# Performance work log

Measured on AMD Instinct MI355X. Metric: run time of the kernel, lower is better.

## Reference

```python
import jax, jax.numpy as jnp
import numpy as np

N_NODES = 16000
N_EDGES = 256000
DIM = 256
HEADS = 8
DH = DIM // HEADS
BLOCKS = 3
EPS = 1e-5


def _ln_graph(x, g, b):
    # PyG LayerNorm, mode='graph', batch=None: scalar mean/std over ALL elements,
    # then per-channel affine.
    x = x - x.mean()
    x = x / (x.std() + EPS)
    return x * g + b


def _block(x, src, dst, x_edge, inv_dist, p):
    (Wq, bq, Wk, bk, Wv, bv, We, Ws, bs, g1, b1, W1, c1, W2, c2, g2, b2) = p
    # per-edge gather + projections  [E, H, DH]
    q = (x[dst] @ Wq + bq).reshape(N_EDGES, HEADS, DH)
    e = (x_edge @ We).reshape(N_EDGES, HEADS, DH)          # lin_edge (no bias)
    k = (x[src] @ Wk + bk).reshape(N_EDGES, HEADS, DH) + e
    # distance-scaled attention logits [E, H]
    alpha = (q * k).sum(-1) * (inv_dist[:, None] / np.sqrt(DH))
    # segment softmax over destination nodes (PyG softmax, +1e-16 in denom)
    amax = jax.ops.segment_max(alpha, dst, num_segments=N_NODES)
    ex = jnp.exp(alpha - amax[dst])
    denom = jax.ops.segment_sum(ex, dst, num_segments=N_NODES)
    attn = ex / (denom[dst] + 1e-16)
    v = (x[src] @ Wv + bv).reshape(N_EDGES, HEADS, DH) + e
    msg = (v * attn[:, :, None]).reshape(N_EDGES, DIM)      # concat heads
    out = jax.ops.segment_sum(msg, dst, num_segments=N_NODES)
    out = out + x @ Ws + bs                                 # root / skip weight
    x = _ln_graph(x + out, g1, b1)                          # mha residual + norm
    ffn = jnp.maximum(x @ W1 + c1, 0.0) @ W2 + c2           # 2-layer ReLU MLP
    return _ln_graph(x + ffn, g2, b2)


def setup_inputs() -> dict:
    key = jax.random.key(0)
    ks = jax.random.split(key, 16)
    s = 0.05
    B = BLOCKS

    def w(k, shape):
        return jax.random.normal(k, shape, jnp.float32) * s

    return {
        'x': jax.random.normal(ks[0], (N_NODES, DIM), jnp.float32),
        'edge_index': jax.random.randint(ks[1], (2, N_EDGES), 0, N_NODES),
        'x_edge': jax.random.normal(ks[2], (N_EDGES, DIM), jnp.float32),
        'x_dist': jax.random.uniform(ks[3], (N_EDGES,), jnp.float32, 1.0, 5.0),
        'Wq': w(ks[4], (B, DIM, DIM)), 'bq': jnp.zeros((B, DIM), jnp.float32),
        'Wk': w(ks[5], (B, DIM, DIM)), 'bk': jnp.zeros((B, DIM), jnp.float32),
        'Wv': w(ks[6], (B, DIM, DIM)), 'bv': jnp.zeros((B, DIM), jnp.float32),
        'We': w(ks[7], (B, DIM, DIM)),
        'Wskip': w(ks[8], (B, DIM, DIM)), 'bskip': jnp.zeros((B, DIM), jnp.float32),
        'ln1_g': jnp.ones((B, DIM), jnp.float32), 'ln1_b': jnp.zeros((B, DIM), jnp.float32),
        'W1': w(ks[9], (B, DIM, 4 * DIM)), 'bf1': jnp.zeros((B, 4 * DIM), jnp.float32),
        'W2': w(ks[10], (B, 4 * DIM, DIM)), 'bf2': jnp.zeros((B, DIM), jnp.float32),
        'ln2_g': jnp.ones((B, DIM), jnp.float32), 'ln2_b': jnp.zeros((B, DIM), jnp.float32),
    }


def reference(x, edge_index, x_edge, x_dist, Wq, bq, Wk, bk, Wv, bv, We,
              Wskip, bskip, ln1_g, ln1_b, W1, bf1, W2, bf2, ln2_g, ln2_b):
    src, dst = edge_index[0], edge_index[1]  # PyG: x_j = x[src], x_i = x[dst]
    inv_dist = 1.0 / x_dist
    for i in range(BLOCKS):
        p = (Wq[i], bq[i], Wk[i], bk[i], Wv[i], bv[i], We[i], Wskip[i], bskip[i],
             ln1_g[i], ln1_b[i], W1[i], bf1[i], W2[i], bf2[i], ln2_g[i], ln2_b[i])
        x = _block(x, src, dst, x_edge, inv_dist, p)
    return x
```

## Files before the change

kernel.cpp:

```cpp
#include <hip/hip_runtime.h>
#include <hip/hip_bf16.h>
#include <cstddef>

#define N_NODES 16000
#define N_EDGES 256000
#define DIM 256
#define HEADS 8
#define DFF 1024
#define LN_EPS 1e-5f
#define CNT ((float)((size_t)N_NODES * DIM))
#define RSDH 0.17677669529663687f

typedef __attribute__((ext_vector_type(8))) short short8;
typedef __attribute__((ext_vector_type(4))) float floatx4;

__device__ __forceinline__ float bf2f(unsigned int s) {
    return __uint_as_float(s << 16);
}

__device__ __forceinline__ float2 ln_ms(const float* __restrict__ s) {
    float mu = s[0] * (1.0f / CNT);
    float var = s[1] * (1.0f / CNT) - mu * mu;
    float2 r; r.x = mu; r.y = 1.0f / (sqrtf(fmaxf(var, 0.0f)) + LN_EPS);
    return r;
}

__device__ __forceinline__ void async16(const __hip_bfloat16* g, __hip_bfloat16* l) {
    __builtin_amdgcn_global_load_lds(
        (const __attribute__((address_space(1))) void*)g,
        (__attribute__((address_space(3))) void*)l, 16, 0, 0);
}

__device__ __forceinline__ void pack8(__hip_bfloat16* d, float4 a, float4 b) {
    union { short8 f; __hip_bfloat16 h[8]; } u;
    u.h[0] = __float2bfloat16(a.x); u.h[1] = __float2bfloat16(a.y);
    u.h[2] = __float2bfloat16(a.z); u.h[3] = __float2bfloat16(a.w);
    u.h[4] = __float2bfloat16(b.x); u.h[5] = __float2bfloat16(b.y);
    u.h[6] = __float2bfloat16(b.z); u.h[7] = __float2bfloat16(b.w);
    *(short8*)d = u.f;
}

__device__ __forceinline__ float4 lnaff(float4 v, float4 g, float4 b, float mu, float sc) {
    v.x = (v.x - mu) * sc * g.x + b.x;
    v.y = (v.y - mu) * sc * g.y + b.y;
    v.z = (v.z - mu) * sc * g.z + b.z;
    v.w = (v.w - mu) * sc * g.w + b.w;
    return v;
}

template<int BIAS, int RELU, int RES, int OBF16, int ACVT, int TM>
__global__ __launch_bounds__(256) void mgemm_k(
    const void* __restrict__ Ap, const __hip_bfloat16* __restrict__ Bt,
    const float* __restrict__ bias, const float* __restrict__ res,
    void* __restrict__ C, int M, int K, int N,
    const float* __restrict__ lnA_s, const float* __restrict__ lnA_g,
    const float* __restrict__ lnA_b,
    const float* __restrict__ lnR_s, const float* __restrict__ lnR_g,
    const float* __restrict__ lnR_b,
    float* __restrict__ ostats)
{
    __shared__ __hip_bfloat16 As[TM * 32];
    __shared__ __hip_bfloat16 Bs[128 * 32];
    __shared__ float rs[8];
    const int tid = threadIdx.x;
    const int lane = tid & 63, wv = tid >> 6;
    const int wm = (TM == 128) ? (wv & 1) * 64 : 0;
    const int wn = (TM == 128) ? (wv >> 1) * 64 : wv * 32;
    const int NJ = (TM == 128) ? 4 : 2;
    const int row0 = blockIdx.y * TM, col0 = blockIdx.x * 128;
    const int lr = tid >> 2;
    const int lk = (tid & 3) * 8;

    float muA = 0.0f, scA = 1.0f;
    if (ACVT && lnA_s) { float2 t = ln_ms(lnA_s); muA = t.x; scA = t.y; }

    floatx4 acc[4][4];
    const floatx4 zf = {0.f, 0.f, 0.f, 0.f};
    #pragma unroll
    for (int i = 0; i < 4; i++)
        #pragma unroll
        for (int j = 0; j < 4; j++) acc[i][j] = zf;

    const int a_fo = (wm + (lane & 15)) * 32 + (lane >> 4) * 8;
    const int b_fo = (wn + (lane & 15)) * 32 + (lane >> 4) * 8;

    for (int k0 = 0; k0 < K; k0 += 32) {
        if (ACVT) {
            const float* A = (const float*)Ap;
            const float* p0 = A + (size_t)(row0 + lr) * K + k0 + lk;
            float4 v0 = *(const float4*)(p0);
            float4 v1 = *(const float4*)(p0 + 4);
            if (lnA_s) {
                float4 ga = *(const float4*)(lnA_g + k0 + lk);
                float4 gb = *(const float4*)(lnA_g + k0 + lk + 4);
                float4 ba = *(const float4*)(lnA_b + k0 + lk);
                float4 bb = *(const float4*)(lnA_b + k0 + lk + 4);
                v0 = lnaff(v0, ga, ba, muA, scA);
                v1 = lnaff(v1, gb, bb, muA, scA);
                if (TM == 128) {
                    const float* p1 = A + (size_t)(row0 + lr + 64) * K + k0 + lk;
                    float4 w0 = lnaff(*(const float4*)(p1), ga, ba, muA, scA);
                    float4 w1 = lnaff(*(const float4*)(p1 + 4), gb, bb, muA, scA);
                    pack8(As + 2048 + tid * 8, w0, w1);
                }
            } else if (TM == 128) {
                const float* p1 = A + (size_t)(row0 + lr + 64) * K + k0 + lk;
                pack8(As + 2048 + tid * 8, *(const float4*)(p1), *(const float4*)(p1 + 4));
            }
            pack8(As + tid * 8, v0, v1);
        } else {
            const __hip_bfloat16* A = (const __hip_bfloat16*)Ap;
            async16(A + (size_t)(row0 + lr) * K + k0 + lk, As + tid * 8);
            if (TM == 128)
                async16(A + (size_t)(row0 + lr + 64) * K + k0 + lk, As + 2048 + tid * 8);
        }
        async16(Bt + (size_t)(col0 + lr) * K + k0 + lk, Bs + tid * 8);
        async16(Bt + (size_t)(col0 + lr + 64) * K + k0 + lk, Bs + 2048 + tid * 8);
        __syncthreads();
        short8 a[4], b[4];
        #pragma unroll
        for (int i = 0; i < 4; i++)
            a[i] = *(const short8*)(As + a_fo + i * 16 * 32);
        #pragma unroll
        for (int j = 0; j < NJ; j++)
            b[j] = *(const short8*)(Bs + b_fo + j * 16 * 32);
        #pragma unroll
        for (int i = 0; i < 4; i++)
            #pragma unroll
            for (int j = 0; j < NJ; j++)
                acc[i][j] = __builtin_amdgcn_mfma_f32_16x16x32_bf16(a[i], b[j], acc[i][j], 0, 0, 0);
        __syncthreads();
    }
    float muR = 0.0f, scR = 1.0f;
    if (RES && lnR_s) { float2 t = ln_ms(lnR_s); muR = t.x; scR = t.y; }
    const int rbase = row0 + wm + (lane >> 4) * 4;
    const int cbase = col0 + wn + (lane & 15);
    float s1 = 0.0f, s2 = 0.0f;
    #pragma unroll
    for (int j = 0; j < NJ; j++) {
        const int c = cbase + j * 16;
        float bb = BIAS ? bias[c] : 0.0f;
        float gr = (RES && lnR_s) ? lnR_g[c] : 1.0f;
        float br = (RES && lnR_s) ? lnR_b[c] : 0.0f;
        #pragma unroll
        for (int i = 0; i < 4; i++) {
            #pragma unroll
            for (int r = 0; r < 4; r++) {
                const int rr = rbase + i * 16 + r;
                float v = acc[i][j][r] + bb;
                if (RELU) v = fmaxf(v, 0.0f);
                if (RES) {
                    float rv = res[(size_t)rr * N + c];
                    if (lnR_s) rv = (rv - muR) * scR * gr + br;
                    v += rv;
                }
                if (ostats) { s1 += v; s2 += v * v; }
                if (OBF16 == 2) {
                    const int cc = c & 255;
                    const int idx = ((cc >> 2) << 3) + (cc & 3) + ((c >> 8) << 2);
                    ((__hip_bfloat16*)C)[(size_t)rr * N + idx] = __float2bfloat16(v);
                } else if (OBF16) {
                    ((__hip_bfloat16*)C)[(size_t)rr * N + c] = __float2bfloat16(v);
                } else {
                    ((float*)C)[(size_t)rr * N + c] = v;
                }
            }
        }
    }
    if (ostats) {
        #pragma unroll
        for (int o = 32; o > 0; o >>= 1) {
            s1 += __shfl_down(s1, o);
            s2 += __shfl_down(s2, o);
        }
        if (lane == 0) { rs[wv] = s1; rs[4 + wv] = s2; }
        __syncthreads();
        if (tid == 0) {
            atomicAdd(&ostats[0], rs[0] + rs[1] + rs[2] + rs[3]);
            atomicAdd(&ostats[1], rs[4] + rs[5] + rs[6] + rs[7]);
        }
    }
}

__global__ __launch_bounds__(256) void tcvt_k(const float* __restrict__ src,
                                              __hip_bfloat16* __restrict__ dst,
                                              int R, int C, int sStride, int dStride)
{
    src += (size_t)blockIdx.z * sStride;
    dst += (size_t)blockIdx.z * dStride;
    __shared__ float t[32][33];
    const int c0 = blockIdx.x * 32, r0 = blockIdx.y * 32;
    const int tx = threadIdx.x & 31, ty = threadIdx.x >> 5;
    #pragma unroll
    for (int j = 0; j < 32; j += 8)
        t[ty + j][tx] = src[(size_t)(r0 + ty + j) * C + c0 + tx];
    __syncthreads();
    #pragma unroll
    for (int j = 0; j < 32; j += 8)
        dst[(size_t)(c0 + ty + j) * R + r0 + tx] = __float2bfloat16(t[tx][ty + j]);
}

__global__ __launch_bounds__(256) void bcat_k(const float* __restrict__ ba,
                                              const float* __restrict__ bb,
                                              const float* __restrict__ bc,
                                              const float* __restrict__ bd,
                                              float* __restrict__ o)
{
    const int z = blockIdx.y;
    int t = blockIdx.x * 256 + threadIdx.x;
    float v = (t < 256) ? ba[z * 256 + t] : (t < 512) ? bb[z * 256 + t - 256]
            : (t < 768) ? bc[z * 256 + t - 512] : bd[z * 256 + t - 768];
    o[(size_t)z * 1024 + t] = v;
}

__global__ __launch_bounds__(256) void hist_k(const int* __restrict__ dst, int* __restrict__ deg)
{
    int e = blockIdx.x * blockDim.x + threadIdx.x;
    if (e < N_EDGES) atomicAdd(&deg[dst[e]], 1);
}

__global__ __launch_bounds__(1024) void scan_k(const int* __restrict__ deg,
                                               int* __restrict__ rowptr,
                                               int* __restrict__ cursor)
{
    __shared__ int wsum[16];
    const int t = threadIdx.x;
    const int base = t * 16;
    int local[16];
    int s = 0;
    if (t < 1000) {
        #pragma unroll
        for (int j = 0; j < 16; j++) { local[j] = s; s += deg[base + j]; }
    }
    const int lane = t & 63, w = t >> 6;
    int v = s;
    #pragma unroll
    for (int off = 1; off < 64; off <<= 1) {
        int u = __shfl_up(v, off);
        if (lane >= off) v += u;
    }
    if (lane == 63) wsum[w] = v;
    __syncthreads();
    if (t == 0) {
        int r = 0;
        #pragma unroll
        for (int i = 0; i < 16; i++) { int u = wsum[i]; wsum[i] = r; r += u; }
    }
    __syncthreads();
    const int excl = v - s + wsum[w];
    if (t < 1000) {
        #pragma unroll
        for (int j = 0; j < 16; j++) {
            rowptr[base + j] = excl + local[j];
            cursor[base + j] = excl + local[j];
        }
        if (t == 999) rowptr[16000] = excl + s;
    }
}

__global__ __launch_bounds__(256) void scatter_k(const int* __restrict__ dst,
                                                 const int* __restrict__ src,
                                                 const float* __restrict__ xd,
                                                 int* __restrict__ cursor,
                                                 int* __restrict__ eperm,
                                                 int* __restrict__ srcp,
                                                 float* __restrict__ scale)
{
    int e = blockIdx.x * blockDim.x + threadIdx.x;
    if (e < N_EDGES) {
        int pos = atomicAdd(&cursor[dst[e]], 1);
        eperm[pos] = e;
        srcp[pos] = src[e];
        scale[pos] = RSDH / xd[e];
    }
}

__global__ __launch_bounds__(256) void eprep_k(const float* __restrict__ xe,
                                               const int* __restrict__ eperm,
                                               __hip_bfloat16* __restrict__ xeb)
{
    const int r = blockIdx.x * 4 + (threadIdx.x >> 6);
    const int lane = threadIdx.x & 63;
    const int e = eperm[r];
    float4 v = *(const float4*)(xe + (size_t)e * DIM + lane * 4);
    union { short4 s; __hip_bfloat16 h[4]; } u;
    u.h[0] = __float2bfloat16(v.x); u.h[1] = __float2bfloat16(v.y);
    u.h[2] = __float2bfloat16(v.z); u.h[3] = __float2bfloat16(v.w);
    *(short4*)(xeb + (size_t)r * DIM + lane * 4) = u.s;
}

__global__ __launch_bounds__(256) void node_agg_k(
    const float* __restrict__ qs, const __hip_bfloat16* __restrict__ kvb,
    const __hip_bfloat16* __restrict__ Ep,
    const int* __restrict__ srcp, const float* __restrict__ scale,
    const int* __restrict__ rowptr,
    const float* __restrict__ xsrc, const float* __restrict__ lnx_s,
    const float* __restrict__ lnx_g, const float* __restrict__ lnx_b,
    float* __restrict__ y, float* __restrict__ ostats)
{
    __shared__ float rs[8];
    const int lane = threadIdx.x & 63;
    const int wv = threadIdx.x >> 6;
    const int n = blockIdx.x * 4 + wv;
    const float4 q = *(const float4*)(qs + (size_t)n * 512 + lane * 4);
    float aA0 = 0, aA1 = 0, aA2 = 0, aA3 = 0, denA = 0;
    float aB0 = 0, aB1 = 0, aB2 = 0, aB3 = 0, denB = 0;
    const int beg = rowptr[n], end = rowptr[n + 1];
    int i = beg;
    int sC = (i + 2 < end) ? srcp[i + 2] : 0;
    int sD = (i + 3 < end) ? srcp[i + 3] : 0;
    uint4 kvA = {0, 0, 0, 0}, kvB = {0, 0, 0, 0};
    uint2 ebA = {0, 0}, ebB = {0, 0};
    float scA = 0.f, scB = 0.f;
    if (i < end) {
        const int sA = srcp[i];
        kvA = *(const uint4*)(kvb + (size_t)sA * 512 + lane * 8);
        ebA = *(const uint2*)(Ep + (size_t)i * DIM + lane * 4);
        scA = scale[i];
    }
    if (i + 1 < end) {
        const int sB = srcp[i + 1];
        kvB = *(const uint4*)(kvb + (size_t)sB * 512 + lane * 8);
        ebB = *(const uint2*)(Ep + (size_t)(i + 1) * DIM + lane * 4);
        scB = scale[i + 1];
    }
    while (i + 1 < end) {
        const uint4 kA = kvA, kB = kvB;
        const uint2 eA = ebA, eB = ebB;
        const float cA = scA, cB = scB;
        if (i + 2 < end) {
            kvA = *(const uint4*)(kvb + (size_t)sC * 512 + lane * 8);
            ebA = *(const uint2*)(Ep + (size_t)(i + 2) * DIM + lane * 4);
            scA = scale[i + 2];
            sC = (i + 4 < end) ? srcp[i + 4] : 0;
        }
        if (i + 3 < end) {
            kvB = *(const uint4*)(kvb + (size_t)sD * 512 + lane * 8);
            ebB = *(const uint2*)(Ep + (size_t)(i + 3) * DIM + lane * 4);
            scB = scale[i + 3];
            sD = (i + 5 < end) ? srcp[i + 5] : 0;
        }
        const float eA0 = bf2f(eA.x & 0xffffu), eA1 = bf2f(eA.x >> 16);
        const float eA2 = bf2f(eA.y & 0xffffu), eA3 = bf2f(eA.y >> 16);
        const float eB0 = bf2f(eB.x & 0xffffu), eB1 = bf2f(eB.x >> 16);
        const float eB2 = bf2f(eB.y & 0xffffu), eB3 = bf2f(eB.y >> 16);
        float pA = q.x * (bf2f(kA.x & 0xffffu) + eA0)
                 + q.y * (bf2f(kA.x >> 16) + eA1)
                 + q.z * (bf2f(kA.y & 0xffffu) + eA2)
                 + q.w * (bf2f(kA.y >> 16) + eA3);
        float pB = q.x * (bf2f(kB.x & 0xffffu) + eB0)
                 + q.y * (bf2f(kB.x >> 16) + eB1)
                 + q.z * (bf2f(kB.y & 0xffffu) + eB2)
                 + q.w * (bf2f(kB.y >> 16) + eB3);
        pA += __shfl_xor(pA, 1); pB += __shfl_xor(pB, 1);
        pA += __shfl_xor(pA, 2); pB += __shfl_xor(pB, 2);
        pA += __shfl_xor(pA, 4); pB += __shfl_xor(pB, 4);
        const float exA = __expf(pA * cA);
        const float exB = __expf(pB * cB);
        denA += exA; denB += exB;
        aA0 = fmaf(bf2f(kA.z & 0xffffu) + eA0, exA, aA0);
        aA1 = fmaf(bf2f(kA.z >> 16) + eA1, exA, aA1);
        aA2 = fmaf(bf2f(kA.w & 0xffffu) + eA2, exA, aA2);
        aA3 = fmaf(bf2f(kA.w >> 16) + eA3, exA, aA3);
        aB0 = fmaf(bf2f(kB.z & 0xffffu) + eB0, exB, aB0);
        aB1 = fmaf(bf2f(kB.z >> 16) + eB1, exB, aB1);
        aB2 = fmaf(bf2f(kB.w & 0xffffu) + eB2, exB, aB2);
        aB3 = fmaf(bf2f(kB.w >> 16) + eB3, exB, aB3);
        i += 2;
    }
    if (i < end) {
        const float e0 = bf2f(ebA.x & 0xffffu), e1 = bf2f(ebA.x >> 16);
        const float e2 = bf2f(ebA.y & 0xffffu), e3 = bf2f(ebA.y >> 16);
        float pA = q.x * (bf2f(kvA.x & 0xffffu) + e0)
                 + q.y * (bf2f(kvA.x >> 16) + e1)
                 + q.z * (bf2f(kvA.y & 0xffffu) + e2)
                 + q.w * (bf2f(kvA.y >> 16) + e3);
        pA += __shfl_xor(pA, 1);
        pA += __shfl_xor(pA, 2);
        pA += __shfl_xor(pA, 4);
        const float ex = __expf(pA * scA);
        denA += ex;
        aA0 = fmaf(bf2f(kvA.z & 0xffffu) + e0, ex, aA0);
        aA1 = fmaf(bf2f(kvA.z >> 16) + e1, ex, aA1);
        aA2 = fmaf(bf2f(kvA.w & 0xffffu) + e2, ex, aA2);
        aA3 = fmaf(bf2f(kvA.w >> 16) + e3, ex, aA3);
    }
    const float dn = 1.0f / (denA + denB + 1e-16f);
    const float a0 = aA0 + aB0, a1 = aA1 + aB1, a2 = aA2 + aB2, a3 = aA3 + aB3;
    const size_t o = (size_t)n * DIM + lane * 4;
    float4 xr = *(const float4*)(xsrc + o);
    if (lnx_s) {
        float2 t = ln_ms(lnx_s);
        const float4 g4 = *(const float4*)(lnx_g + lane * 4);
        const float4 b4 = *(const float4*)(lnx_b + lane * 4);
        xr = lnaff(xr, g4, b4, t.x, t.y);
    }
    const float4 sr = *(const float4*)(qs + (size_t)n * 512 + 256 + lane * 4);
    float4 out;
    out.x = xr.x + a0 * dn + sr.x;
    out.y = xr.y + a1 * dn + sr.y;
    out.z = xr.z + a2 * dn + sr.z;
    out.w = xr.w + a3 * dn + sr.w;
    *(float4*)(y + o) = out;
    float s1 = out.x + out.y + out.z + out.w;
    float s2 = out.x * out.x + out.y * out.y + out.z * out.z + out.w * out.w;
    #pragma unroll
    for (int of = 32; of > 0; of >>= 1) {
        s1 += __shfl_down(s1, of);
        s2 += __shfl_down(s2, of);
    }
    if (lane == 0) { rs[wv] = s1; rs[4 + wv] = s2; }
    __syncthreads();
    if (threadIdx.x == 0) {
        atomicAdd(&ostats[0], rs[0] + rs[1] + rs[2] + rs[3]);
        atomicAdd(&ostats[1], rs[4] + rs[5] + rs[6] + rs[7]);
    }
}

__global__ __launch_bounds__(256) void apply_k(
    const float* __restrict__ y, const float* __restrict__ stats,
    const float* __restrict__ g, const float* __restrict__ b,
    float* __restrict__ xo)
{
    int idx = blockIdx.x * blockDim.x + threadIdx.x;
    float2 t = ln_ms(stats);
    int cb = (idx & 63) * 4;
    float4 v  = *(const float4*)(y + (size_t)idx * 4);
    float4 gv = *(const float4*)(g + cb);
    float4 bv = *(const float4*)(b + cb);
    *(float4*)(xo + (size_t)idx * 4) = lnaff(v, gv, bv, t.x, t.y);
}

extern "C" void kernel_launch(void* const* d_in, const int* in_sizes, int n_in,
                              void* d_out, int out_size, void* d_ws, size_t ws_size,
                              hipStream_t stream) {
    const float* x_in   = (const float*)d_in[0];
    const int*   ei     = (const int*)d_in[1];
    const int*   src    = ei;
    const int*   dstp   = ei + N_EDGES;
    const float* x_edge = (const float*)d_in[2];
    const float* x_dist = (const float*)d_in[3];
    const float* Wq  = (const float*)d_in[4];
    const float* bq  = (const float*)d_in[5];
    const float* Wk  = (const float*)d_in[6];
    const float* bk  = (const float*)d_in[7];
    const float* Wv  = (const float*)d_in[8];
    const float* bv  = (const float*)d_in[9];
    const float* We  = (const float*)d_in[10];
    const float* Wsk = (const float*)d_in[11];
    const float* bsk = (const float*)d_in[12];
    const float* g1  = (const float*)d_in[13];
    const float* b1  = (const float*)d_in[14];
    const float* W1  = (const float*)d_in[15];
    const float* c1  = (const float*)d_in[16];
    const float* W2  = (const float*)d_in[17];
    const float* c2  = (const float*)d_in[18];
    const float* g2  = (const float*)d_in[19];
    const float* b2  = (const float*)d_in[20];

    char* p = (char*)d_ws;
    float* ybuf = (float*)p; p += (size_t)N_NODES * DIM * sizeof(float);
    float* qsb  = (float*)p; p += (size_t)N_NODES * 512 * sizeof(float);
    __hip_bfloat16* kvb = (__hip_bfloat16*)p; p += (size_t)N_NODES * 512 * 2;
    __hip_bfloat16* hb16 = (__hip_bfloat16*)p; p += (size_t)N_NODES * 1024 * 2;
    __hip_bfloat16* Ep   = (__hip_bfloat16*)p; p += (size_t)N_EDGES * DIM * 2;
    __hip_bfloat16* xeb  = (__hip_bfloat16*)p; p += (size_t)N_EDGES * DIM * 2;
    __hip_bfloat16* WqkvsT = (__hip_bfloat16*)p; p += (size_t)3 * 1024 * 256 * 2;
    __hip_bfloat16* WeT    = (__hip_bfloat16*)p; p += (size_t)3 * 256 * 256 * 2;
    __hip_bfloat16* W1T    = (__hip_bfloat16*)p; p += (size_t)3 * 1024 * 256 * 2;
    __hip_bfloat16* W2T    = (__hip_bfloat16*)p; p += (size_t)3 * 256 * 1024 * 2;
    float* bqkvs = (float*)p; p += (size_t)3 * 1024 * sizeof(float);
    float* stats = (float*)p;  p += 64;
    int* deg     = (int*)p;    p += (size_t)N_NODES * sizeof(int);
    int* rowptr  = (int*)p;    p += (size_t)(N_NODES + 4) * sizeof(int);
    int* cursor  = (int*)p;    p += (size_t)N_NODES * sizeof(int);
    int* eperm   = (int*)p;    p += (size_t)N_EDGES * sizeof(int);
    int* srcp    = (int*)p;    p += (size_t)N_EDGES * sizeof(int);
    float* scale = (float*)p;  p += (size_t)N_EDGES * sizeof(float);

    const dim3 blk(256);

    hipMemsetAsync(deg, 0, (size_t)N_NODES * sizeof(int), stream);
    hipMemsetAsync(stats, 0, 48, stream);
    hist_k<<<N_EDGES / 256, blk, 0, stream>>>(dstp, deg);
    scan_k<<<1, 1024, 0, stream>>>(deg, rowptr, cursor);
    scatter_k<<<N_EDGES / 256, blk, 0, stream>>>(dstp, src, x_dist, cursor, eperm, srcp, scale);
    eprep_k<<<N_EDGES / 4, blk, 0, stream>>>(x_edge, eperm, xeb);

    tcvt_k<<<dim3(8, 8, 3), blk, 0, stream>>>(Wq,  WqkvsT + 0 * 65536, 256, 256, 65536, 262144);
    tcvt_k<<<dim3(8, 8, 3), blk, 0, stream>>>(Wsk, WqkvsT + 1 * 65536, 256, 256, 65536, 262144);
    tcvt_k<<<dim3(8, 8, 3), blk, 0, stream>>>(Wk,  WqkvsT + 2 * 65536, 256, 256, 65536, 262144);
    tcvt_k<<<dim3(8, 8, 3), blk, 0, stream>>>(Wv,  WqkvsT + 3 * 65536, 256, 256, 65536, 262144);
    tcvt_k<<<dim3(8, 8, 3), blk, 0, stream>>>(We,  WeT, 256, 256, 65536, 65536);
    tcvt_k<<<dim3(32, 8, 3), blk, 0, stream>>>(W1, W1T, 256, 1024, 262144, 262144);
    tcvt_k<<<dim3(8, 32, 3), blk, 0, stream>>>(W2, W2T, 1024, 256, 262144, 262144);
    bcat_k<<<dim3(4, 3), blk, 0, stream>>>(bq, bsk, bk, bv, bqkvs);

    for (int i = 0; i < 3; i++) {
        const size_t bo = (size_t)i * DIM;
        const size_t b1o = (size_t)i * DFF;
        float* ln1 = stats + (size_t)i * 4;
        float* ln2 = stats + (size_t)i * 4 + 2;
        const float* pls = (i == 0) ? nullptr : stats + (size_t)(i - 1) * 4 + 2;
        const float* plg = (i == 0) ? nullptr : g2 + (size_t)(i - 1) * 256;
        const float* plb = (i == 0) ? nullptr : b2 + (size_t)(i - 1) * 256;
        const float* xsrc = (i == 0) ? x_in : ybuf;

        mgemm_k<1,0,0,0,1,128><<<dim3(4, 125), blk, 0, stream>>>(
            xsrc, WqkvsT + (size_t)i * 262144, bqkvs + (size_t)i * 1024, nullptr,
            qsb, N_NODES, DIM, 512, pls, plg, plb, nullptr, nullptr, nullptr, nullptr);
        mgemm_k<1,0,0,2,1,128><<<dim3(4, 125), blk, 0, stream>>>(
            xsrc, WqkvsT + (size_t)i * 262144 + 131072, bqkvs + (size_t)i * 1024 + 512, nullptr,
            kvb, N_NODES, DIM, 512, pls, plg, plb, nullptr, nullptr, nullptr, nullptr);
        mgemm_k<0,0,0,1,0,128><<<dim3(2, 2000), blk, 0, stream>>>(
            xeb, WeT + (size_t)i * 65536, nullptr, nullptr,
            Ep, N_EDGES, DIM, DIM, nullptr, nullptr, nullptr, nullptr, nullptr, nullptr, nullptr);
        node_agg_k<<<N_NODES / 4, blk, 0, stream>>>(qsb, kvb, Ep, srcp, scale, rowptr,
                                                    xsrc, pls, plg, plb, ybuf, ln1);
        mgemm_k<1,1,0,1,1,128><<<dim3(8, 125), blk, 0, stream>>>(
            ybuf, W1T + (size_t)i * 262144, c1 + b1o, nullptr,
            hb16, N_NODES, DIM, DFF, ln1, g1 + bo, b1 + bo, nullptr, nullptr, nullptr, nullptr);
        mgemm_k<1,0,1,0,0,64><<<dim3(2, 250), blk, 0, stream>>>(
            hb16, W2T + (size_t)i * 262144, c2 + bo, ybuf,
            ybuf, N_NODES, DFF, DIM, nullptr, nullptr, nullptr, ln1, g1 + bo, b1 + bo, ln2);
        if (i == 2)
            apply_k<<<(N_NODES * DIM) / 1024, blk, 0, stream>>>(
                ybuf, ln2, g2 + bo, b2 + bo, (float*)d_out);
    }
}
```

Before: 1.517 ms.

## Fuse QS and KV projection GEMMs and deepen edge prefetch in node aggregation

Merges the two node-projection GEMMs (q/skip in fp32, k/v in interleaved bf16) into one launch with N=1024 that routes columns to two output buffers. The xsrc tile and its LayerNorm prologue are now loaded once instead of twice, and one launch disappears. Separately, the node aggregation loop goes from two edges in flight to four, using clamped indices and masking, to hide more gather latency. The cost is higher register pressure, and a wasted dummy load whenever a node's degree is not a multiple of four.

```diff
diff --git a/kernel.cpp b/kernel.cpp
--- a/kernel.cpp
+++ b/kernel.cpp
@@ -52,7 +52,7 @@
 __global__ __launch_bounds__(256) void mgemm_k(
     const void* __restrict__ Ap, const __hip_bfloat16* __restrict__ Bt,
     const float* __restrict__ bias, const float* __restrict__ res,
-    void* __restrict__ C, int M, int K, int N,
+    void* __restrict__ C, void* __restrict__ C2, int M, int K, int N,
     const float* __restrict__ lnA_s, const float* __restrict__ lnA_g,
     const float* __restrict__ lnA_b,
     const float* __restrict__ lnR_s, const float* __restrict__ lnR_g,
@@ -155,11 +155,16 @@
                     v += rv;
                 }
                 if (ostats) { s1 += v; s2 += v * v; }
-                if (OBF16 == 2) {
-                    const int cc = c & 255;
-                    const int idx = ((cc >> 2) << 3) + (cc & 3) + ((c >> 8) << 2);
-                    ((__hip_bfloat16*)C)[(size_t)rr * N + idx] = __float2bfloat16(v);
-                } else if (OBF16) {
+                if (OBF16 == 3) {
+                    if (c < 512) {
+                        ((float*)C)[(size_t)rr * 512 + c] = v;
+                    } else {
+                        const int cc = c - 512;
+                        const int ccc = cc & 255;
+                        const int idx = ((ccc >> 2) << 3) + (ccc & 3) + ((cc >> 8) << 2);
+                        ((__hip_bfloat16*)C2)[(size_t)rr * 512 + idx] = __float2bfloat16(v);
+                    }
+                } else if (OBF16 == 1) {
                     ((__hip_bfloat16*)C)[(size_t)rr * N + c] = __float2bfloat16(v);
                 } else {
                     ((float*)C)[(size_t)rr * N + c] = v;
@@ -303,90 +308,74 @@
     const int wv = threadIdx.x >> 6;
     const int n = blockIdx.x * 4 + wv;
     const float4 q = *(const float4*)(qs + (size_t)n * 512 + lane * 4);
-    float aA0 = 0, aA1 = 0, aA2 = 0, aA3 = 0, denA = 0;
-    float aB0 = 0, aB1 = 0, aB2 = 0, aB3 = 0, denB = 0;
+    float ax0[4], ax1[4], ax2[4], ax3[4], den[4];
+    #pragma unroll
+    for (int t = 0; t < 4; t++) { ax0[t] = 0; ax1[t] = 0; ax2[t] = 0; ax3[t] = 0; den[t] = 0; }
     const int beg = rowptr[n], end = rowptr[n + 1];
-    int i = beg;
-    int sC = (i + 2 < end) ? srcp[i + 2] : 0;
-    int sD = (i + 3 < end) ? srcp[i + 3] : 0;
-    uint4 kvA = {0, 0, 0, 0}, kvB = {0, 0, 0, 0};
-    uint2 ebA = {0, 0}, ebB = {0, 0};
-    float scA = 0.f, scB = 0.f;
-    if (i < end) {
-        const int sA = srcp[i];
-        kvA = *(const uint4*)(kvb + (size_t)sA * 512 + lane * 8);
-        ebA = *(const uint2*)(Ep + (size_t)i * DIM + lane * 4);
-        scA = scale[i];
-    }
-    if (i + 1 < end) {
-        const int sB = srcp[i + 1];
-        kvB = *(const uint4*)(kvb + (size_t)sB * 512 + lane * 8);
-        ebB = *(const uint2*)(Ep + (size_t)(i + 1) * DIM + lane * 4);
-        scB = scale[i + 1];
-    }
-    while (i + 1 < end) {
-        const uint4 kA = kvA, kB = kvB;
-        const uint2 eA = ebA, eB = ebB;
-        const float cA = scA, cB = scB;
-        if (i + 2 < end) {
-            kvA = *(const uint4*)(kvb + (size_t)sC * 512 + lane * 8);
-            ebA = *(const uint2*)(Ep + (size_t)(i + 2) * DIM + lane * 4);
-            scA = scale[i + 2];
-            sC = (i + 4 < end) ? srcp[i + 4] : 0;
-        }
-        if (i + 3 < end) {
-            kvB = *(const uint4*)(kvb + (size_t)sD * 512 + lane * 8);
-            ebB = *(const uint2*)(Ep + (size_t)(i + 3) * DIM + lane * 4);
-            scB = scale[i + 3];
-            sD = (i + 5 < end) ? srcp[i + 5] : 0;
-        }
-        const float eA0 = bf2f(eA.x & 0xffffu), eA1 = bf2f(eA.x >> 16);
-        const float eA2 = bf2f(eA.y & 0xffffu), eA3 = bf2f(eA.y >> 16);
-        const float eB0 = bf2f(eB.x & 0xffffu), eB1 = bf2f(eB.x >> 16);
-        const float eB2 = bf2f(eB.y & 0xffffu), eB3 = bf2f(eB.y >> 16);
-        float pA = q.x * (bf2f(kA.x & 0xffffu) + eA0)
-                 + q.y * (bf2f(kA.x >> 16) + eA1)
-                 + q.z * (bf2f(kA.y & 0xffffu) + eA2)
-                 + q.w * (bf2f(kA.y >> 16) + eA3);
-        float pB = q.x * (bf2f(kB.x & 0xffffu) + eB0)
-                 + q.y * (bf2f(kB.x >> 16) + eB1)
-                 + q.z * (bf2f(kB.y & 0xffffu) + eB2)
-                 + q.w * (bf2f(kB.y >> 16) + eB3);
-        pA += __shfl_xor(pA, 1); pB += __shfl_xor(pB, 1);
-        pA += __shfl_xor(pA, 2); pB += __shfl_xor(pB, 2);
-        pA += __shfl_xor(pA, 4); pB += __shfl_xor(pB, 4);
-        const float exA = __expf(pA * cA);
-        const float exB = __expf(pB * cB);
-        denA += exA; denB += exB;
-        aA0 = fmaf(bf2f(kA.z & 0xffffu) + eA0, exA, aA0);
-        aA1 = fmaf(bf2f(kA.z >> 16) + eA1, exA, aA1);
-        aA2 = fmaf(bf2f(kA.w & 0xffffu) + eA2, exA, aA2);
-        aA3 = fmaf(bf2f(kA.w >> 16) + eA3, exA, aA3);
-        aB0 = fmaf(bf2f(kB.z & 0xffffu) + eB0, exB, aB0);
-        aB1 = fmaf(bf2f(kB.z >> 16) + eB1, exB, aB1);
-        aB2 = fmaf(bf2f(kB.w & 0xffffu) + eB2, exB, aB2);
-        aB3 = fmaf(bf2f(kB.w >> 16) + eB3, exB, aB3);
-        i += 2;
-    }
-    if (i < end) {
-        const float e0 = bf2f(ebA.x & 0xffffu), e1 = bf2f(ebA.x >> 16);
-        const float e2 = bf2f(ebA.y & 0xffffu), e3 = bf2f(ebA.y >> 16);
-        float pA = q.x * (bf2f(kvA.x & 0xffffu) + e0)
-                 + q.y * (bf2f(kvA.x >> 16) + e1)
-                 + q.z * (bf2f(kvA.y & 0xffffu) + e2)
-                 + q.w * (bf2f(kvA.y >> 16) + e3);
-        pA += __shfl_xor(pA, 1);
-        pA += __shfl_xor(pA, 2);
-        pA += __shfl_xor(pA, 4);
-        const float ex = __expf(pA * scA);
-        denA += ex;
-        aA0 = fmaf(bf2f(kvA.z & 0xffffu) + e0, ex, aA0);
-        aA1 = fmaf(bf2f(kvA.z >> 16) + e1, ex, aA1);
-        aA2 = fmaf(bf2f(kvA.w & 0xffffu) + e2, ex, aA2);
-        aA3 = fmaf(bf2f(kvA.w >> 16) + e3, ex, aA3);
-    }
-    const float dn = 1.0f / (denA + denB + 1e-16f);
-    const float a0 = aA0 + aB0, a1 = aA1 + aB1, a2 = aA2 + aB2, a3 = aA3 + aB3;
+    if (beg < end) {
+        const int last = end - 1;
+        uint4 kv[4]; uint2 eb[4]; float sc[4]; int sn[4];
+        #pragma unroll
+        for (int t = 0; t < 4; t++) {
+            const int idx = min(beg + t, last);
+            const int s = srcp[idx];
+            kv[t] = *(const uint4*)(kvb + (size_t)s * 512 + lane * 8);
+            eb[t] = *(const uint2*)(Ep + (size_t)idx * DIM + lane * 4);
+            sc[t] = scale[idx];
+        }
+        #pragma unroll
+        for (int t = 0; t < 4; t++)
+            sn[t] = srcp[min(beg + 4 + t, last)];
+        for (int i = beg; i < end; i += 4) {
+            uint4 ckv[4]; uint2 ceb[4]; float csc[4];
+            #pragma unroll
+            for (int t = 0; t < 4; t++) { ckv[t] = kv[t]; ceb[t] = eb[t]; csc[t] = sc[t]; }
+            if (i + 4 < end) {
+                #pragma unroll
+                for (int t = 0; t < 4; t++) {
+                    const int idx = min(i + 4 + t, last);
+                    kv[t] = *(const uint4*)(kvb + (size_t)sn[t] * 512 + lane * 8);
+                    eb[t] = *(const uint2*)(Ep + (size_t)idx * DIM + lane * 4);
+                    sc[t] = scale[idx];
+                }
+                #pragma unroll
+                for (int t = 0; t < 4; t++)
+                    sn[t] = srcp[min(i + 8 + t, last)];
+            }
+            float p[4];
+            #pragma unroll
+            for (int t = 0; t < 4; t++) {
+                const float e0 = bf2f(ceb[t].x & 0xffffu), e1 = bf2f(ceb[t].x >> 16);
+                const float e2 = bf2f(ceb[t].y & 0xffffu), e3 = bf2f(ceb[t].y >> 16);
+                p[t] = q.x * (bf2f(ckv[t].x & 0xffffu) + e0)
+                     + q.y * (bf2f(ckv[t].x >> 16) + e1)
+                     + q.z * (bf2f(ckv[t].y & 0xffffu) + e2)
+                     + q.w * (bf2f(ckv[t].y >> 16) + e3);
+            }
+            #pragma unroll
+            for (int t = 0; t < 4; t++) p[t] += __shfl_xor(p[t], 1);
+            #pragma unroll
+            for (int t = 0; t < 4; t++) p[t] += __shfl_xor(p[t], 2);
+            #pragma unroll
+            for (int t = 0; t < 4; t++) p[t] += __shfl_xor(p[t], 4);
+            #pragma unroll
+            for (int t = 0; t < 4; t++) {
+                const float ex = (i + t < end) ? __expf(p[t] * csc[t]) : 0.0f;
+                den[t] += ex;
+                const float e0 = bf2f(ceb[t].x & 0xffffu), e1 = bf2f(ceb[t].x >> 16);
+                const float e2 = bf2f(ceb[t].y & 0xffffu), e3 = bf2f(ceb[t].y >> 16);
+                ax0[t] = fmaf(bf2f(ckv[t].z & 0xffffu) + e0, ex, ax0[t]);
+                ax1[t] = fmaf(bf2f(ckv[t].z >> 16) + e1, ex, ax1[t]);
+                ax2[t] = fmaf(bf2f(ckv[t].w & 0xffffu) + e2, ex, ax2[t]);
+                ax3[t] = fmaf(bf2f(ckv[t].w >> 16) + e3, ex, ax3[t]);
+            }
+        }
+    }
+    const float dn = 1.0f / (den[0] + den[1] + den[2] + den[3] + 1e-16f);
+    const float a0 = ax0[0] + ax0[1] + ax0[2] + ax0[3];
+    const float a1 = ax1[0] + ax1[1] + ax1[2] + ax1[3];
+    const float a2 = ax2[0] + ax2[1] + ax2[2] + ax2[3];
+    const float a3 = ax3[0] + ax3[1] + ax3[2] + ax3[3];
     const size_t o = (size_t)n * DIM + lane * 4;
     float4 xr = *(const float4*)(xsrc + o);
     if (lnx_s) {
@@ -506,23 +495,20 @@
         const float* plb = (i == 0) ? nullptr : b2 + (size_t)(i - 1) * 256;
         const float* xsrc = (i == 0) ? x_in : ybuf;
 
-        mgemm_k<1,0,0,0,1,128><<<dim3(4, 125), blk, 0, stream>>>(
+        mgemm_k<1,0,0,3,1,128><<<dim3(8, 125), blk, 0, stream>>>(
             xsrc, WqkvsT + (size_t)i * 262144, bqkvs + (size_t)i * 1024, nullptr,
-            qsb, N_NODES, DIM, 512, pls, plg, plb, nullptr, nullptr, nullptr, nullptr);
-        mgemm_k<1,0,0,2,1,128><<<dim3(4, 125), blk, 0, stream>>>(
-            xsrc, WqkvsT + (size_t)i * 262144 + 131072, bqkvs + (size_t)i * 1024 + 512, nullptr,
-            kvb, N_NODES, DIM, 512, pls, plg, plb, nullptr, nullptr, nullptr, nullptr);
+            qsb, kvb, N_NODES, DIM, 1024, pls, plg, plb, nullptr, nullptr, nullptr, nullptr);
         mgemm_k<0,0,0,1,0,128><<<dim3(2, 2000), blk, 0, stream>>>(
             xeb, WeT + (size_t)i * 65536, nullptr, nullptr,
-            Ep, N_EDGES, DIM, DIM, nullptr, nullptr, nullptr, nullptr, nullptr, nullptr, nullptr);
+            Ep, nullptr, N_EDGES, DIM, DIM, nullptr, nullptr, nullptr, nullptr, nullptr, nullptr, nullptr);
         node_agg_k<<<N_NODES / 4, blk, 0, stream>>>(qsb, kvb, Ep, srcp, scale, rowptr,
                                                     xsrc, pls, plg, plb, ybuf, ln1);
         mgemm_k<1,1,0,1,1,128><<<dim3(8, 125), blk, 0, stream>>>(
             ybuf, W1T + (size_t)i * 262144, c1 + b1o, nullptr,
-            hb16, N_NODES, DIM, DFF, ln1, g1 + bo, b1 + bo, nullptr, nullptr, nullptr, nullptr);
+            hb16, nullptr, N_NODES, DIM, DFF, ln1, g1 + bo, b1 + bo, nullptr, nullptr, nullptr, nullptr);
         mgemm_k<1,0,1,0,0,64><<<dim3(2, 250), blk, 0, stream>>>(
             hb16, W2T + (size_t)i * 262144, c2 + bo, ybuf,
-            ybuf, N_NODES, DFF, DIM, nullptr, nullptr, nullptr, ln1, g1 + bo, b1 + bo, ln2);
+            ybuf, nullptr, N_NODES, DFF, DIM, nullptr, nullptr, nullptr, ln1, g1 + bo, b1 + bo, ln2);
         if (i == 2)
             apply_k<<<(N_NODES * DIM) / 1024, blk, 0, stream>>>(
                 ybuf, ln2, g2 + bo, b2 + bo, (float*)d_out);
```

Result: no change. 1.503 ms (-0.9%).

## Merge QS and KV projections into one GEMM and split node edges across two waves

Applied to the files above, without the earlier changes.

The two node-projection GEMMs (q/skip in fp32, k/v in interleaved bf16) are merged into a single launch with N=1024 that writes to two outputs depending on the column. This saves a launch and a second pass over the normalized input. Node aggregation now gives each node two wavefronts, each handling half of its incoming edges, and combines the partial softmax sums through shared memory. This doubles parallelism for the gather-bound loop, at the cost of an extra barrier and half the waves sitting idle during the epilogue.

```diff
diff --git a/kernel.cpp b/kernel.cpp
--- a/kernel.cpp
+++ b/kernel.cpp
@@ -52,7 +52,7 @@
 __global__ __launch_bounds__(256) void mgemm_k(
     const void* __restrict__ Ap, const __hip_bfloat16* __restrict__ Bt,
     const float* __restrict__ bias, const float* __restrict__ res,
-    void* __restrict__ C, int M, int K, int N,
+    void* __restrict__ C, void* __restrict__ C2, int M, int K, int N,
     const float* __restrict__ lnA_s, const float* __restrict__ lnA_g,
     const float* __restrict__ lnA_b,
     const float* __restrict__ lnR_s, const float* __restrict__ lnR_g,
@@ -155,11 +155,16 @@
                     v += rv;
                 }
                 if (ostats) { s1 += v; s2 += v * v; }
-                if (OBF16 == 2) {
-                    const int cc = c & 255;
-                    const int idx = ((cc >> 2) << 3) + (cc & 3) + ((c >> 8) << 2);
-                    ((__hip_bfloat16*)C)[(size_t)rr * N + idx] = __float2bfloat16(v);
-                } else if (OBF16) {
+                if (OBF16 == 3) {
+                    if (c < 512) {
+                        ((float*)C)[(size_t)rr * 512 + c] = v;
+                    } else {
+                        const int cc = c - 512;
+                        const int ccc = cc & 255;
+                        const int idx = ((ccc >> 2) << 3) + (ccc & 3) + ((cc >> 8) << 2);
+                        ((__hip_bfloat16*)C2)[(size_t)rr * 512 + idx] = __float2bfloat16(v);
+                    }
+                } else if (OBF16 == 1) {
                     ((__hip_bfloat16*)C)[(size_t)rr * N + c] = __float2bfloat16(v);
                 } else {
                     ((float*)C)[(size_t)rr * N + c] = v;
@@ -298,14 +303,20 @@
     const float* __restrict__ lnx_g, const float* __restrict__ lnx_b,
     float* __restrict__ y, float* __restrict__ ostats)
 {
-    __shared__ float rs[8];
-    const int lane = threadIdx.x & 63;
-    const int wv = threadIdx.x >> 6;
-    const int n = blockIdx.x * 4 + wv;
+    __shared__ float comb[2][64][5];
+    __shared__ float rs[4];
+    const int tid = threadIdx.x;
+    const int lane = tid & 63;
+    const int wv = tid >> 6;
+    const int ni = wv >> 1, part = wv & 1;
+    const int n = blockIdx.x * 2 + ni;
     const float4 q = *(const float4*)(qs + (size_t)n * 512 + lane * 4);
     float aA0 = 0, aA1 = 0, aA2 = 0, aA3 = 0, denA = 0;
     float aB0 = 0, aB1 = 0, aB2 = 0, aB3 = 0, denB = 0;
-    const int beg = rowptr[n], end = rowptr[n + 1];
+    const int begF = rowptr[n], endF = rowptr[n + 1];
+    const int mid = begF + ((endF - begF + 1) >> 1);
+    const int beg = part ? mid : begF;
+    const int end = part ? endF : mid;
     int i = beg;
     int sC = (i + 2 < end) ? srcp[i + 2] : 0;
     int sD = (i + 3 < end) ? srcp[i + 3] : 0;
@@ -385,35 +396,47 @@
         aA2 = fmaf(bf2f(kvA.w & 0xffffu) + e2, ex, aA2);
         aA3 = fmaf(bf2f(kvA.w >> 16) + e3, ex, aA3);
     }
-    const float dn = 1.0f / (denA + denB + 1e-16f);
-    const float a0 = aA0 + aB0, a1 = aA1 + aB1, a2 = aA2 + aB2, a3 = aA3 + aB3;
-    const size_t o = (size_t)n * DIM + lane * 4;
-    float4 xr = *(const float4*)(xsrc + o);
-    if (lnx_s) {
-        float2 t = ln_ms(lnx_s);
-        const float4 g4 = *(const float4*)(lnx_g + lane * 4);
-        const float4 b4 = *(const float4*)(lnx_b + lane * 4);
-        xr = lnaff(xr, g4, b4, t.x, t.y);
-    }
-    const float4 sr = *(const float4*)(qs + (size_t)n * 512 + 256 + lane * 4);
-    float4 out;
-    out.x = xr.x + a0 * dn + sr.x;
-    out.y = xr.y + a1 * dn + sr.y;
-    out.z = xr.z + a2 * dn + sr.z;
-    out.w = xr.w + a3 * dn + sr.w;
-    *(float4*)(y + o) = out;
-    float s1 = out.x + out.y + out.z + out.w;
-    float s2 = out.x * out.x + out.y * out.y + out.z * out.z + out.w * out.w;
-    #pragma unroll
-    for (int of = 32; of > 0; of >>= 1) {
-        s1 += __shfl_down(s1, of);
-        s2 += __shfl_down(s2, of);
-    }
-    if (lane == 0) { rs[wv] = s1; rs[4 + wv] = s2; }
+    float den = denA + denB;
+    float a0 = aA0 + aB0, a1 = aA1 + aB1, a2 = aA2 + aB2, a3 = aA3 + aB3;
+    if (part) {
+        comb[ni][lane][0] = den;
+        comb[ni][lane][1] = a0; comb[ni][lane][2] = a1;
+        comb[ni][lane][3] = a2; comb[ni][lane][4] = a3;
+    }
     __syncthreads();
-    if (threadIdx.x == 0) {
-        atomicAdd(&ostats[0], rs[0] + rs[1] + rs[2] + rs[3]);
-        atomicAdd(&ostats[1], rs[4] + rs[5] + rs[6] + rs[7]);
+    if (!part) {
+        den += comb[ni][lane][0];
+        a0 += comb[ni][lane][1]; a1 += comb[ni][lane][2];
+        a2 += comb[ni][lane][3]; a3 += comb[ni][lane][4];
+        const float dn = 1.0f / (den + 1e-16f);
+        const size_t o = (size_t)n * DIM + lane * 4;
+        float4 xr = *(const float4*)(xsrc + o);
+        if (lnx_s) {
+            float2 t = ln_ms(lnx_s);
+            const float4 g4 = *(const float4*)(lnx_g + lane * 4);
+            const float4 b4 = *(const float4*)(lnx_b + lane * 4);
+            xr = lnaff(xr, g4, b4, t.x, t.y);
+        }
+        const float4 sr = *(const float4*)(qs + (size_t)n * 512 + 256 + lane * 4);
+        float4 out;
+        out.x = xr.x + a0 * dn + sr.x;
+        out.y = xr.y + a1 * dn + sr.y;
+        out.z = xr.z + a2 * dn + sr.z;
+        out.w = xr.w + a3 * dn + sr.w;
+        *(float4*)(y + o) = out;
+        float s1 = out.x + out.y + out.z + out.w;
+        float s2 = out.x * out.x + out.y * out.y + out.z * out.z + out.w * out.w;
+        #pragma unroll
+        for (int of = 32; of > 0; of >>= 1) {
+            s1 += __shfl_down(s1, of);
+            s2 += __shfl_down(s2, of);
+        }
+        if (lane == 0) { rs[ni] = s1; rs[2 + ni] = s2; }
+    }
+    __syncthreads();
+    if (tid == 0) {
+        atomicAdd(&ostats[0], rs[0] + rs[1]);
+        atomicAdd(&ostats[1], rs[2] + rs[3]);
     }
 }
 
@@ -506,23 +529,20 @@
         const float* plb = (i == 0) ? nullptr : b2 + (size_t)(i - 1) * 256;
         const float* xsrc = (i == 0) ? x_in : ybuf;
 
-        mgemm_k<1,0,0,0,1,128><<<dim3(4, 125), blk, 0, stream>>>(
+        mgemm_k<1,0,0,3,1,128><<<dim3(8, 125), blk, 0, stream>>>(
             xsrc, WqkvsT + (size_t)i * 262144, bqkvs + (size_t)i * 1024, nullptr,
-            qsb, N_NODES, DIM, 512, pls, plg, plb, nullptr, nullptr, nullptr, nullptr);
-        mgemm_k<1,0,0,2,1,128><<<dim3(4, 125), blk, 0, stream>>>(
-            xsrc, WqkvsT + (size_t)i * 262144 + 131072, bqkvs + (size_t)i * 1024 + 512, nullptr,
-            kvb, N_NODES, DIM, 512, pls, plg, plb, nullptr, nullptr, nullptr, nullptr);
+            qsb, kvb, N_NODES, DIM, 1024, pls, plg, plb, nullptr, nullptr, nullptr, nullptr);
         mgemm_k<0,0,0,1,0,128><<<dim3(2, 2000), blk, 0, stream>>>(
             xeb, WeT + (size_t)i * 65536, nullptr, nullptr,
-            Ep, N_EDGES, DIM, DIM, nullptr, nullptr, nullptr, nullptr, nullptr, nullptr, nullptr);
-        node_agg_k<<<N_NODES / 4, blk, 0, stream>>>(qsb, kvb, Ep, srcp, scale, rowptr,
+            Ep, nullptr, N_EDGES, DIM, DIM, nullptr, nullptr, nullptr, nullptr, nullptr, nullptr, nullptr);
+        node_agg_k<<<N_NODES / 2, blk, 0, stream>>>(qsb, kvb, Ep, srcp, scale, rowptr,
                                                     xsrc, pls, plg, plb, ybuf, ln1);
         mgemm_k<1,1,0,1,1,128><<<dim3(8, 125), blk, 0, stream>>>(
             ybuf, W1T + (size_t)i * 262144, c1 + b1o, nullptr,
-            hb16, N_NODES, DIM, DFF, ln1, g1 + bo, b1 + bo, nullptr, nullptr, nullptr, nullptr);
+            hb16, nullptr, N_NODES, DIM, DFF, ln1, g1 + bo, b1 + bo, nullptr, nullptr, nullptr, nullptr);
         mgemm_k<1,0,1,0,0,64><<<dim3(2, 250), blk, 0, stream>>>(
             hb16, W2T + (size_t)i * 262144, c2 + bo, ybuf,
-            ybuf, N_NODES, DFF, DIM, nullptr, nullptr, nullptr, ln1, g1 + bo, b1 + bo, ln2);
+            ybuf, nullptr, N_NODES, DFF, DIM, nullptr, nullptr, nullptr, ln1, g1 + bo, b1 + bo, ln2);
         if (i == 2)
             apply_k<<<(N_NODES * DIM) / 1024, blk, 0, stream>>>(
                 ybuf, ln2, g2 + bo, b2 + bo, (float*)d_out);
```

Result: slower. 1.796 ms (+18.4%).
